# Performance work log

Measured on AMD Instinct MI355X. Metric: run time of the kernel, lower is better.

Reference implementation:

```python
import jax, jax.numpy as jnp
import numpy as np

EPS = 1e-6

def setup_inputs() -> dict:
    key = jax.random.key(0)
    ks = jax.random.split(key, 6)
    N, E, Din, H, D = 50000, 800000, 256, 4, 32
    x = jax.random.normal(ks[0], (N, Din), dtype=jnp.float32)
    adj_indices = jax.random.randint(ks[1], (E, 2), 0, N, dtype=jnp.int32)
    adj_weights = jax.random.uniform(ks[2], (E,), dtype=jnp.float32)
    W = jax.random.normal(ks[3], (Din, H * D), dtype=jnp.float32) * (1.0 / np.sqrt(Din))
    a_src = jax.random.normal(ks[4], (H, D), dtype=jnp.float32)
    a_dst = jax.random.normal(ks[5], (H, D), dtype=jnp.float32)
    return {"x": x, "adj_indices": adj_indices, "adj_weights": adj_weights,
            "W": W, "a_src": a_src, "a_dst": a_dst}

def reference(x, adj_indices, adj_weights, W, a_src, a_dst):
    N = x.shape[0]
    H, D = a_src.shape
    h = (x @ W).reshape(N, H, D)                       # [N,H,D]
    src = adj_indices[:, 0]
    dst = adj_indices[:, 1]
    hs = h[src]                                        # [E,H,D]
    hd = h[dst]                                        # [E,H,D]
    raw = jnp.einsum('ehd,hd->eh', hs, a_src) + jnp.einsum('ehd,hd->eh', hd, a_dst)
    gate = jnp.clip(adj_weights, EPS, None)[:, None]   # [E,1]
    scores = jnp.tanh(raw) + jnp.log(gate)             # [E,H]
    # per-destination segment softmax (numerically stable)
    seg_max = jax.ops.segment_max(scores, dst, num_segments=N)   # [N,H]
    ex = jnp.exp(scores - seg_max[dst])
    denom = jax.ops.segment_sum(ex, dst, num_segments=N)         # [N,H]
    alpha = ex / denom[dst]                            # softmax over edges per dst
    alpha = alpha * gate
    messages = alpha[:, :, None] * hs                  # [E,H,D]
    out = jax.ops.segment_sum(messages, dst, num_segments=N)     # [N,H,D]
    out = out.reshape(N, H * D)
    return jax.nn.gelu(out, approximate=False)
```

## Files before the change

### kernel.cpp

```cpp
#include <hip/hip_runtime.h>
#include <hip/hip_bf16.h>

#define N_NODES 50000
#define N_EDGES 800000
#define DIN 256
#define HD 128
#define NH 4
#define CAP 64
#define NSH 8
#define SCAP 16

#define GROWS 64
#define LDKH 136

#define GEMM_BLOCKS ((N_NODES + GROWS - 1) / GROWS)
#define SCAT_BLOCKS ((N_EDGES + 255) / 256)

typedef __bf16 bf16x8 __attribute__((ext_vector_type(8)));
typedef float  f32x4  __attribute__((ext_vector_type(4)));

static __device__ __forceinline__ unsigned short f2bu(float v) {
  union { __hip_bfloat16 b; unsigned short u; } c;
  c.b = __float2bfloat16(v);
  return c.u;
}

static __device__ __forceinline__ unsigned short f2hu(float v) {
  union { _Float16 h; unsigned short u; } c;
  c.h = (_Float16)v;
  return c.u;
}

static __device__ __forceinline__ float hu2f(unsigned short u) {
  union { _Float16 h; unsigned short u; } c;
  c.u = u;
  return (float)c.h;
}

__global__ void init_kernel(const float* __restrict__ W,
                            unsigned short* __restrict__ WtF) {
  int i = blockIdx.x * 256 + threadIdx.x;
  if (i < HD * DIN) {
    int j    = i & 7;
    int lane = (i >> 3) & 63;
    int t    = (i >> 9) & 7;
    int s    = (i >> 12) & 3;
    int ks   = (i >> 14) & 1;
    int m = lane & 15, q = lane >> 4;
    int k = ks * 128 + 32 * s + 8 * q + j;
    int c = 16 * t + m;
    WtF[i] = f2bu(W[k * HD + c]);
  }
}

__global__ __launch_bounds__(256, 4) void scatter_kernel(
    const int2* __restrict__ adj,
    const float* __restrict__ wts,
    int* __restrict__ cursor_s,
    unsigned int* __restrict__ slots_s) {
  int e = blockIdx.x * 256 + threadIdx.x;
  if (e >= N_EDGES) return;
  const int shard = blockIdx.x & (NSH - 1);
  int2 sd = adj[e];
  if ((unsigned)sd.x >= (unsigned)N_NODES || (unsigned)sd.y >= (unsigned)N_NODES) return;
  float g = fmaxf(wts[e], 1e-6f);
  int pos = atomicAdd(&cursor_s[shard * N_NODES + sd.y], 1);
  if (pos >= SCAP) pos = SCAP - 1;
  unsigned packed = ((unsigned)f2hu(g) << 16) | (unsigned)(sd.x & 0xffff);
  slots_s[((size_t)shard * N_NODES + sd.y) * SCAP + pos] = packed;
}

__global__ __launch_bounds__(256, 2) void gemm_kernel(
    const float* __restrict__ x,
    const unsigned short* __restrict__ WtF,
    const float* __restrict__ a_src,
    const float* __restrict__ a_dst,
    unsigned short* __restrict__ hbf,
    float* __restrict__ ssrc,
    float* __restrict__ sdst) {
  __shared__ unsigned short xs[GROWS * LDKH];
  const int tid = threadIdx.x;

  const int row0 = blockIdx.x * GROWS;
  const int wid  = tid >> 6;
  const int lane = tid & 63;
  const int m    = lane & 15;
  const int q    = lane >> 4;

  float4 v0[8];
#pragma unroll
  for (int it = 0; it < 8; it++) {
    int i = it * 256 + tid, r = i >> 5, kq = i & 31;
    int row = row0 + r;
    v0[it] = (row < N_NODES) ? *(const float4*)(x + (size_t)row * DIN + 4 * kq)
                             : make_float4(0.f, 0.f, 0.f, 0.f);
  }
#pragma unroll
  for (int it = 0; it < 8; it++) {
    int i = it * 256 + tid, r = i >> 5, kq = i & 31;
    ushort4 b;
    b.x = f2bu(v0[it].x); b.y = f2bu(v0[it].y); b.z = f2bu(v0[it].z); b.w = f2bu(v0[it].w);
    *(ushort4*)&xs[r * LDKH + 4 * kq] = b;
  }
  __syncthreads();

  f32x4 acc[8];
#pragma unroll
  for (int t = 0; t < 8; t++) acc[t] = (f32x4){0.f, 0.f, 0.f, 0.f};

  const unsigned short* xbase = &xs[(wid * 16 + m) * LDKH];

  bf16x8 a0[4];
#pragma unroll
  for (int s = 0; s < 4; s++) a0[s] = *(const bf16x8*)(xbase + 32 * s + 8 * q);

  float4 v1[8];
#pragma unroll
  for (int it = 0; it < 8; it++) {
    int i = it * 256 + tid, r = i >> 5, kq = i & 31;
    int row = row0 + r;
    v1[it] = (row < N_NODES) ? *(const float4*)(x + (size_t)row * DIN + 128 + 4 * kq)
                             : make_float4(0.f, 0.f, 0.f, 0.f);
  }

#pragma unroll
  for (int s = 0; s < 4; s++) {
    bf16x8 bfr[8];
#pragma unroll
    for (int t = 0; t < 8; t++)
      bfr[t] = *(const bf16x8*)(WtF + (size_t)((0 * 4 + s) * 8 + t) * 512 + lane * 8);
#pragma unroll
    for (int t = 0; t < 8; t++)
      acc[t] = __builtin_amdgcn_mfma_f32_16x16x32_bf16(a0[s], bfr[t], acc[t], 0, 0, 0);
  }
  __syncthreads();

#pragma unroll
  for (int it = 0; it < 8; it++) {
    int i = it * 256 + tid, r = i >> 5, kq = i & 31;
    ushort4 b;
    b.x = f2bu(v1[it].x); b.y = f2bu(v1[it].y); b.z = f2bu(v1[it].z); b.w = f2bu(v1[it].w);
    *(ushort4*)&xs[r * LDKH + 4 * kq] = b;
  }
  __syncthreads();

  bf16x8 a1[4];
#pragma unroll
  for (int s = 0; s < 4; s++) a1[s] = *(const bf16x8*)(xbase + 32 * s + 8 * q);

#pragma unroll
  for (int s = 0; s < 4; s++) {
    bf16x8 bfr[8];
#pragma unroll
    for (int t = 0; t < 8; t++)
      bfr[t] = *(const bf16x8*)(WtF + (size_t)((1 * 4 + s) * 8 + t) * 512 + lane * 8);
#pragma unroll
    for (int t = 0; t < 8; t++)
      acc[t] = __builtin_amdgcn_mfma_f32_16x16x32_bf16(a1[s], bfr[t], acc[t], 0, 0, 0);
  }

#pragma unroll
  for (int t = 0; t < 8; t++) {
#pragma unroll
    for (int r = 0; r < 4; r++) {
      int row = row0 + wid * 16 + q * 4 + r;
      if (row < N_NODES) hbf[(size_t)row * HD + 16 * t + m] = f2bu(acc[t][r]);
    }
  }

  float as[8], ad[8];
#pragma unroll
  for (int t = 0; t < 8; t++) {
    as[t] = a_src[16 * t + m];
    ad[t] = a_dst[16 * t + m];
  }
#pragma unroll
  for (int r = 0; r < 4; r++) {
    float ps[NH] = {0.f, 0.f, 0.f, 0.f};
    float pd[NH] = {0.f, 0.f, 0.f, 0.f};
#pragma unroll
    for (int t = 0; t < 8; t++) {
      ps[t >> 1] = fmaf(acc[t][r], as[t], ps[t >> 1]);
      pd[t >> 1] = fmaf(acc[t][r], ad[t], pd[t >> 1]);
    }
#pragma unroll
    for (int mm = 8; mm >= 1; mm >>= 1) {
#pragma unroll
      for (int hh = 0; hh < NH; hh++) {
        ps[hh] += __shfl_xor(ps[hh], mm, 64);
        pd[hh] += __shfl_xor(pd[hh], mm, 64);
      }
    }
    int row = row0 + wid * 16 + q * 4 + r;
    if (m == 0 && row < N_NODES) {
#pragma unroll
      for (int hh = 0; hh < NH; hh++) {
        ssrc[row * NH + hh] = ps[hh];
        sdst[row * NH + hh] = pd[hh];
      }
    }
  }
}

__global__ __launch_bounds__(128, 4) void node_kernel(
    const int* __restrict__ cursor_s,
    const unsigned int* __restrict__ slots_s,
    const float4* __restrict__ ssrc4,
    const float4* __restrict__ sdst4,
    const unsigned int* __restrict__ hbf32,
    float* __restrict__ out) {
  const int tid  = threadIdx.x;
  const int wid  = tid >> 6;
  const int lane = tid & 63;
  const int n    = blockIdx.x * 2 + wid;
  const int hh   = lane >> 4;

  __shared__ unsigned spk[2][CAP];
  __shared__ int    sidx[2][CAP];
  __shared__ float4 swv[2][CAP];

  int c[NSH], o[NSH];
  int tot = 0;
#pragma unroll
  for (int s = 0; s < NSH; s++) {
    int cs = cursor_s[s * N_NODES + n];
    cs = (cs < SCAP) ? cs : SCAP;
    c[s] = cs;
    o[s] = tot;
    tot += cs;
  }
  const int deg = (tot < CAP) ? tot : CAP;
#pragma unroll
  for (int s = 0; s < NSH; s++) {
    if (lane < c[s]) {
      int d = o[s] + lane;
      if (d < CAP)
        spk[wid][d] = slots_s[((size_t)s * N_NODES + n) * SCAP + lane];
    }
  }
  __syncthreads();

  float4 ex = make_float4(0.f, 0.f, 0.f, 0.f);
  if (lane < deg) {
    unsigned sl = spk[wid][lane];
    int s = (int)(sl & 0xffffu);
    float g = hu2f((unsigned short)(sl >> 16));
    float4 ss = ssrc4[s];
    float4 sd = sdst4[n];
    ex.x = g * expf(tanhf(ss.x + sd.x));
    ex.y = g * expf(tanhf(ss.y + sd.y));
    ex.z = g * expf(tanhf(ss.z + sd.z));
    ex.w = g * expf(tanhf(ss.w + sd.w));
    sidx[wid][lane] = s;
    swv[wid][lane] = make_float4(ex.x * g, ex.y * g, ex.z * g, ex.w * g);
  }

  float4 tot4 = ex;
#pragma unroll
  for (int mm = 32; mm >= 1; mm >>= 1) {
    tot4.x += __shfl_xor(tot4.x, mm, 64);
    tot4.y += __shfl_xor(tot4.y, mm, 64);
    tot4.z += __shfl_xor(tot4.z, mm, 64);
    tot4.w += __shfl_xor(tot4.w, mm, 64);
  }
  float dn  = (hh == 0) ? tot4.x : (hh == 1) ? tot4.y : (hh == 2) ? tot4.z : tot4.w;
  float inv = (dn > 0.f) ? 1.f / dn : 0.f;
  __syncthreads();

  float acc0 = 0.f, acc1 = 0.f;
  int j = 0;
  for (; j + 8 <= deg; j += 8) {
    int s0 = sidx[wid][j + 0], s1 = sidx[wid][j + 1];
    int s2 = sidx[wid][j + 2], s3 = sidx[wid][j + 3];
    int s4 = sidx[wid][j + 4], s5 = sidx[wid][j + 5];
    int s6 = sidx[wid][j + 6], s7 = sidx[wid][j + 7];
    unsigned u0 = hbf32[(size_t)s0 * (HD / 2) + lane];
    unsigned u1 = hbf32[(size_t)s1 * (HD / 2) + lane];
    unsigned u2 = hbf32[(size_t)s2 * (HD / 2) + lane];
    unsigned u3 = hbf32[(size_t)s3 * (HD / 2) + lane];
    unsigned u4 = hbf32[(size_t)s4 * (HD / 2) + lane];
    unsigned u5 = hbf32[(size_t)s5 * (HD / 2) + lane];
    unsigned u6 = hbf32[(size_t)s6 * (HD / 2) + lane];
    unsigned u7 = hbf32[(size_t)s7 * (HD / 2) + lane];
    float w0 = ((const float*)&swv[wid][j + 0])[hh];
    float w1 = ((const float*)&swv[wid][j + 1])[hh];
    float w2 = ((const float*)&swv[wid][j + 2])[hh];
    float w3 = ((const float*)&swv[wid][j + 3])[hh];
    float w4 = ((const float*)&swv[wid][j + 4])[hh];
    float w5 = ((const float*)&swv[wid][j + 5])[hh];
    float w6 = ((const float*)&swv[wid][j + 6])[hh];
    float w7 = ((const float*)&swv[wid][j + 7])[hh];
    acc0 = fmaf(w0, __uint_as_float(u0 << 16), acc0);
    acc1 = fmaf(w0, __uint_as_float(u0 & 0xffff0000u), acc1);
    acc0 = fmaf(w1, __uint_as_float(u1 << 16), acc0);
    acc1 = fmaf(w1, __uint_as_float(u1 & 0xffff0000u), acc1);
    acc0 = fmaf(w2, __uint_as_float(u2 << 16), acc0);
    acc1 = fmaf(w2, __uint_as_float(u2 & 0xffff0000u), acc1);
    acc0 = fmaf(w3, __uint_as_float(u3 << 16), acc0);
    acc1 = fmaf(w3, __uint_as_float(u3 & 0xffff0000u), acc1);
    acc0 = fmaf(w4, __uint_as_float(u4 << 16), acc0);
    acc1 = fmaf(w4, __uint_as_float(u4 & 0xffff0000u), acc1);
    acc0 = fmaf(w5, __uint_as_float(u5 << 16), acc0);
    acc1 = fmaf(w5, __uint_as_float(u5 & 0xffff0000u), acc1);
    acc0 = fmaf(w6, __uint_as_float(u6 << 16), acc0);
    acc1 = fmaf(w6, __uint_as_float(u6 & 0xffff0000u), acc1);
    acc0 = fmaf(w7, __uint_as_float(u7 << 16), acc0);
    acc1 = fmaf(w7, __uint_as_float(u7 & 0xffff0000u), acc1);
  }
  for (; j < deg; j++) {
    int s0 = sidx[wid][j];
    unsigned u0 = hbf32[(size_t)s0 * (HD / 2) + lane];
    float w0 = ((const float*)&swv[wid][j])[hh];
    acc0 = fmaf(w0, __uint_as_float(u0 << 16), acc0);
    acc1 = fmaf(w0, __uint_as_float(u0 & 0xffff0000u), acc1);
  }
  acc0 *= inv;
  acc1 *= inv;

  float2 gl;
  gl.x = 0.5f * acc0 * (1.f + erff(acc0 * 0.70710678118654752f));
  gl.y = 0.5f * acc1 * (1.f + erff(acc1 * 0.70710678118654752f));
  *(float2*)&out[(size_t)n * HD + 2 * lane] = gl;
}

extern "C" void kernel_launch(void* const* d_in, const int* in_sizes, int n_in,
                              void* d_out, int out_size, void* d_ws, size_t ws_size,
                              hipStream_t stream) {
  const float* x     = (const float*)d_in[0];
  const int2*  adj   = (const int2*)d_in[1];
  const float* wts   = (const float*)d_in[2];
  const float* W     = (const float*)d_in[3];
  const float* a_src = (const float*)d_in[4];
  const float* a_dst = (const float*)d_in[5];
  float* out = (float*)d_out;

  char* p = (char*)d_ws;
  auto carve = [&](size_t bytes) {
    char* q = p;
    p += (bytes + 255) & ~(size_t)255;
    return (void*)q;
  };
  unsigned short* hbf = (unsigned short*)carve((size_t)N_NODES * HD * sizeof(unsigned short));
  unsigned short* WtF = (unsigned short*)carve((size_t)HD * DIN * sizeof(unsigned short));
  float* ssrc   = (float*)carve((size_t)N_NODES * NH * sizeof(float));
  float* sdst   = (float*)carve((size_t)N_NODES * NH * sizeof(float));
  unsigned int* slots_s = (unsigned int*)carve((size_t)NSH * N_NODES * SCAP * sizeof(unsigned int));
  int* cursor_s = (int*)carve((size_t)NSH * N_NODES * sizeof(int));

  hipMemsetAsync(cursor_s, 0, (size_t)NSH * N_NODES * sizeof(int), stream);
  init_kernel<<<(HD * DIN + 255) / 256, 256, 0, stream>>>(W, WtF);
  scatter_kernel<<<SCAT_BLOCKS, 256, 0, stream>>>(adj, wts, cursor_s, slots_s);
  gemm_kernel<<<GEMM_BLOCKS, 256, 0, stream>>>(x, WtF, a_src, a_dst, hbf, ssrc, sdst);
  node_kernel<<<N_NODES / 2, 128, 0, stream>>>(cursor_s, slots_s, (const float4*)ssrc,
                                               (const float4*)sdst,
                                               (const unsigned int*)hbf, out);
}
```

Before: 230.4 us.

## Fuse scatter into GEMM launch, fold cursor memset into init, parallelize node scoring

The cursor zeroing moves out of a separate memset and into the init kernel. The edge-scatter work runs as extra blocks of the GEMM launch, so the two independent phases can overlap and one launch is removed. In the node kernel, edge scoring is spread over all lanes, one edge-head pair per lane. It uses a fast exp-based tanh with one shared-memory weight array and reuses the packed slots instead of a separate index array. This trades launch overhead and serialized per-lane transcendental work for a heterogeneous block mix in the fused kernel, and for small accuracy differences from __expf.

```diff
diff --git a/kernel.cpp b/kernel.cpp
--- a/kernel.cpp
+++ b/kernel.cpp
@@ -15,6 +15,7 @@
 
 #define GEMM_BLOCKS ((N_NODES + GROWS - 1) / GROWS)
 #define SCAT_BLOCKS ((N_EDGES + 255) / 256)
+#define INIT_ITEMS  (NSH * N_NODES)
 
 typedef __bf16 bf16x8 __attribute__((ext_vector_type(8)));
 typedef float  f32x4  __attribute__((ext_vector_type(4)));
@@ -38,7 +39,8 @@
 }
 
 __global__ void init_kernel(const float* __restrict__ W,
-                            unsigned short* __restrict__ WtF) {
+                            unsigned short* __restrict__ WtF,
+                            int* __restrict__ cursor_s) {
   int i = blockIdx.x * 256 + threadIdx.x;
   if (i < HD * DIN) {
     int j    = i & 7;
@@ -51,35 +53,37 @@
     int c = 16 * t + m;
     WtF[i] = f2bu(W[k * HD + c]);
   }
-}
-
-__global__ __launch_bounds__(256, 4) void scatter_kernel(
-    const int2* __restrict__ adj,
-    const float* __restrict__ wts,
-    int* __restrict__ cursor_s,
-    unsigned int* __restrict__ slots_s) {
-  int e = blockIdx.x * 256 + threadIdx.x;
-  if (e >= N_EDGES) return;
-  const int shard = blockIdx.x & (NSH - 1);
-  int2 sd = adj[e];
-  if ((unsigned)sd.x >= (unsigned)N_NODES || (unsigned)sd.y >= (unsigned)N_NODES) return;
-  float g = fmaxf(wts[e], 1e-6f);
-  int pos = atomicAdd(&cursor_s[shard * N_NODES + sd.y], 1);
-  if (pos >= SCAP) pos = SCAP - 1;
-  unsigned packed = ((unsigned)f2hu(g) << 16) | (unsigned)(sd.x & 0xffff);
-  slots_s[((size_t)shard * N_NODES + sd.y) * SCAP + pos] = packed;
-}
-
-__global__ __launch_bounds__(256, 2) void gemm_kernel(
+  if (i < INIT_ITEMS) cursor_s[i] = 0;
+}
+
+__global__ __launch_bounds__(256, 2) void fused_gemm_scatter(
     const float* __restrict__ x,
     const unsigned short* __restrict__ WtF,
     const float* __restrict__ a_src,
     const float* __restrict__ a_dst,
     unsigned short* __restrict__ hbf,
     float* __restrict__ ssrc,
-    float* __restrict__ sdst) {
+    float* __restrict__ sdst,
+    const int2* __restrict__ adj,
+    const float* __restrict__ wts,
+    int* __restrict__ cursor_s,
+    unsigned int* __restrict__ slots_s) {
   __shared__ unsigned short xs[GROWS * LDKH];
   const int tid = threadIdx.x;
+
+  if (blockIdx.x >= GEMM_BLOCKS) {
+    int e = (blockIdx.x - GEMM_BLOCKS) * 256 + tid;
+    if (e >= N_EDGES) return;
+    const int shard = blockIdx.x & (NSH - 1);
+    int2 sd = adj[e];
+    if ((unsigned)sd.x >= (unsigned)N_NODES || (unsigned)sd.y >= (unsigned)N_NODES) return;
+    float g = fmaxf(wts[e], 1e-6f);
+    int pos = atomicAdd(&cursor_s[shard * N_NODES + sd.y], 1);
+    if (pos >= SCAP) pos = SCAP - 1;
+    unsigned packed = ((unsigned)f2hu(g) << 16) | (unsigned)(sd.x & 0xffff);
+    slots_s[((size_t)shard * N_NODES + sd.y) * SCAP + pos] = packed;
+    return;
+  }
 
   const int row0 = blockIdx.x * GROWS;
   const int wid  = tid >> 6;
@@ -205,8 +209,8 @@
 __global__ __launch_bounds__(128, 4) void node_kernel(
     const int* __restrict__ cursor_s,
     const unsigned int* __restrict__ slots_s,
-    const float4* __restrict__ ssrc4,
-    const float4* __restrict__ sdst4,
+    const float* __restrict__ ssrc,
+    const float* __restrict__ sdst,
     const unsigned int* __restrict__ hbf32,
     float* __restrict__ out) {
   const int tid  = threadIdx.x;
@@ -214,10 +218,10 @@
   const int lane = tid & 63;
   const int n    = blockIdx.x * 2 + wid;
   const int hh   = lane >> 4;
+  const int hq   = lane & 3;
 
   __shared__ unsigned spk[2][CAP];
-  __shared__ int    sidx[2][CAP];
-  __shared__ float4 swv[2][CAP];
+  __shared__ float    swf[2][CAP * NH];
 
   int c[NSH], o[NSH];
   int tot = 0;
@@ -240,40 +244,37 @@
   }
   __syncthreads();
 
-  float4 ex = make_float4(0.f, 0.f, 0.f, 0.f);
-  if (lane < deg) {
-    unsigned sl = spk[wid][lane];
-    int s = (int)(sl & 0xffffu);
-    float g = hu2f((unsigned short)(sl >> 16));
-    float4 ss = ssrc4[s];
-    float4 sd = sdst4[n];
-    ex.x = g * expf(tanhf(ss.x + sd.x));
-    ex.y = g * expf(tanhf(ss.y + sd.y));
-    ex.z = g * expf(tanhf(ss.z + sd.z));
-    ex.w = g * expf(tanhf(ss.w + sd.w));
-    sidx[wid][lane] = s;
-    swv[wid][lane] = make_float4(ex.x * g, ex.y * g, ex.z * g, ex.w * g);
-  }
-
-  float4 tot4 = ex;
-#pragma unroll
-  for (int mm = 32; mm >= 1; mm >>= 1) {
-    tot4.x += __shfl_xor(tot4.x, mm, 64);
-    tot4.y += __shfl_xor(tot4.y, mm, 64);
-    tot4.z += __shfl_xor(tot4.z, mm, 64);
-    tot4.w += __shfl_xor(tot4.w, mm, 64);
-  }
-  float dn  = (hh == 0) ? tot4.x : (hh == 1) ? tot4.y : (hh == 2) ? tot4.z : tot4.w;
-  float inv = (dn > 0.f) ? 1.f / dn : 0.f;
+  const float sdn = sdst[n * NH + hq];
+  float den = 0.f;
+  for (int base = 0; base < deg; base += 16) {
+    int e = base + (lane >> 2);
+    float exv = 0.f;
+    if (e < deg) {
+      unsigned sl = spk[wid][e];
+      int s = (int)(sl & 0xffffu);
+      float g = hu2f((unsigned short)(sl >> 16));
+      float xx = ssrc[s * NH + hq] + sdn;
+      float t = 1.f - 2.f / (1.f + __expf(2.f * xx));
+      exv = g * __expf(t);
+      swf[wid][e * NH + hq] = exv * g;
+    }
+    den += exv;
+  }
+  den += __shfl_xor(den, 4, 64);
+  den += __shfl_xor(den, 8, 64);
+  den += __shfl_xor(den, 16, 64);
+  den += __shfl_xor(den, 32, 64);
+  float dh  = __shfl(den, hh, 64);
+  float inv = (dh > 0.f) ? 1.f / dh : 0.f;
   __syncthreads();
 
   float acc0 = 0.f, acc1 = 0.f;
   int j = 0;
   for (; j + 8 <= deg; j += 8) {
-    int s0 = sidx[wid][j + 0], s1 = sidx[wid][j + 1];
-    int s2 = sidx[wid][j + 2], s3 = sidx[wid][j + 3];
-    int s4 = sidx[wid][j + 4], s5 = sidx[wid][j + 5];
-    int s6 = sidx[wid][j + 6], s7 = sidx[wid][j + 7];
+    int s0 = (int)(spk[wid][j + 0] & 0xffffu), s1 = (int)(spk[wid][j + 1] & 0xffffu);
+    int s2 = (int)(spk[wid][j + 2] & 0xffffu), s3 = (int)(spk[wid][j + 3] & 0xffffu);
+    int s4 = (int)(spk[wid][j + 4] & 0xffffu), s5 = (int)(spk[wid][j + 5] & 0xffffu);
+    int s6 = (int)(spk[wid][j + 6] & 0xffffu), s7 = (int)(spk[wid][j + 7] & 0xffffu);
     unsigned u0 = hbf32[(size_t)s0 * (HD / 2) + lane];
     unsigned u1 = hbf32[(size_t)s1 * (HD / 2) + lane];
     unsigned u2 = hbf32[(size_t)s2 * (HD / 2) + lane];
@@ -282,14 +283,14 @@
     unsigned u5 = hbf32[(size_t)s5 * (HD / 2) + lane];
     unsigned u6 = hbf32[(size_t)s6 * (HD / 2) + lane];
     unsigned u7 = hbf32[(size_t)s7 * (HD / 2) + lane];
-    float w0 = ((const float*)&swv[wid][j + 0])[hh];
-    float w1 = ((const float*)&swv[wid][j + 1])[hh];
-    float w2 = ((const float*)&swv[wid][j + 2])[hh];
-    float w3 = ((const float*)&swv[wid][j + 3])[hh];
-    float w4 = ((const float*)&swv[wid][j + 4])[hh];
-    float w5 = ((const float*)&swv[wid][j + 5])[hh];
-    float w6 = ((const float*)&swv[wid][j + 6])[hh];
-    float w7 = ((const float*)&swv[wid][j + 7])[hh];
+    float w0 = swf[wid][(j + 0) * NH + hh];
+    float w1 = swf[wid][(j + 1) * NH + hh];
+    float w2 = swf[wid][(j + 2) * NH + hh];
+    float w3 = swf[wid][(j + 3) * NH + hh];
+    float w4 = swf[wid][(j + 4) * NH + hh];
+    float w5 = swf[wid][(j + 5) * NH + hh];
+    float w6 = swf[wid][(j + 6) * NH + hh];
+    float w7 = swf[wid][(j + 7) * NH + hh];
     acc0 = fmaf(w0, __uint_as_float(u0 << 16), acc0);
     acc1 = fmaf(w0, __uint_as_float(u0 & 0xffff0000u), acc1);
     acc0 = fmaf(w1, __uint_as_float(u1 << 16), acc0);
@@ -308,9 +309,9 @@
     acc1 = fmaf(w7, __uint_as_float(u7 & 0xffff0000u), acc1);
   }
   for (; j < deg; j++) {
-    int s0 = sidx[wid][j];
+    int s0 = (int)(spk[wid][j] & 0xffffu);
     unsigned u0 = hbf32[(size_t)s0 * (HD / 2) + lane];
-    float w0 = ((const float*)&swv[wid][j])[hh];
+    float w0 = swf[wid][j * NH + hh];
     acc0 = fmaf(w0, __uint_as_float(u0 << 16), acc0);
     acc1 = fmaf(w0, __uint_as_float(u0 & 0xffff0000u), acc1);
   }
@@ -347,11 +348,9 @@
   unsigned int* slots_s = (unsigned int*)carve((size_t)NSH * N_NODES * SCAP * sizeof(unsigned int));
   int* cursor_s = (int*)carve((size_t)NSH * N_NODES * sizeof(int));
 
-  hipMemsetAsync(cursor_s, 0, (size_t)NSH * N_NODES * sizeof(int), stream);
-  init_kernel<<<(HD * DIN + 255) / 256, 256, 0, stream>>>(W, WtF);
-  scatter_kernel<<<SCAT_BLOCKS, 256, 0, stream>>>(adj, wts, cursor_s, slots_s);
-  gemm_kernel<<<GEMM_BLOCKS, 256, 0, stream>>>(x, WtF, a_src, a_dst, hbf, ssrc, sdst);
-  node_kernel<<<N_NODES / 2, 128, 0, stream>>>(cursor_s, slots_s, (const float4*)ssrc,
-                                               (const float4*)sdst,
+  init_kernel<<<(INIT_ITEMS + 255) / 256, 256, 0, stream>>>(W, WtF, cursor_s);
+  fused_gemm_scatter<<<GEMM_BLOCKS + SCAT_BLOCKS, 256, 0, stream>>>(
+      x, WtF, a_src, a_dst, hbf, ssrc, sdst, adj, wts, cursor_s, slots_s);
+  node_kernel<<<N_NODES / 2, 128, 0, stream>>>(cursor_s, slots_s, ssrc, sdst,
                                                (const unsigned int*)hbf, out);
 }
```

Result: faster. 195.9 us (-15.0%).
